# Performance work log

Hardware: AMD Instinct MI355X
Metric: run time of the kernel (lower is better)

Reference implementation:

```python
import jax, jax.numpy as jnp
import numpy as np

N, H, NH, R, E = 50000, 128, 8, 100, 800000
HD = H // NH  # head_dim = 16


def _linear(x, W, b):
    # torch nn.Linear convention: W is [out, in]
    return x @ W.T + b


def _layernorm(x, g, b, eps=1e-5):
    mu = jnp.mean(x, axis=-1, keepdims=True)
    var = jnp.var(x, axis=-1, keepdims=True)
    return (x - mu) * jax.lax.rsqrt(var + eps) * g + b


def setup_inputs() -> dict:
    key = jax.random.key(0)
    ks = jax.random.split(key, 24)
    s = 0.02
    inp = {
        "node_features": jax.random.normal(ks[0], (N, H), jnp.float32),
        "query_embedding": jax.random.normal(ks[1], (1, H), jnp.float32),
        "edge_index": jax.random.randint(ks[2], (2, E), 0, N),
        "edge_type": jax.random.randint(ks[3], (E,), 0, R),
        "relation_embeddings": jax.random.normal(ks[4], (R, H), jnp.float32),
        # attention params
        "Wq": jax.random.normal(ks[5], (H, 2 * H), jnp.float32) * s,
        "bq": jnp.zeros((H,), jnp.float32),
        "Wk": jax.random.normal(ks[6], (H, 2 * H), jnp.float32) * s,
        "bk": jnp.zeros((H,), jnp.float32),
        "Wv": jax.random.normal(ks[7], (H, H), jnp.float32) * s,
        "bv": jnp.zeros((H,), jnp.float32),
        "Wo": jax.random.normal(ks[8], (H, H), jnp.float32) * s,
        "bo": jnp.zeros((H,), jnp.float32),
        # norms
        "n1g": jnp.ones((H,), jnp.float32), "n1b": jnp.zeros((H,), jnp.float32),
        "n2g": jnp.ones((H,), jnp.float32), "n2b": jnp.zeros((H,), jnp.float32),
        # ffn
        "W1": jax.random.normal(ks[9], (4 * H, H), jnp.float32) * s,
        "b1": jnp.zeros((4 * H,), jnp.float32),
        "W2": jax.random.normal(ks[10], (H, 4 * H), jnp.float32) * s,
        "b2": jnp.zeros((H,), jnp.float32),
        # relational layer: 4 interaction transforms stacked [4, H, H]
        "relW": jax.random.normal(ks[11], (4, H, H), jnp.float32) * s,
        "relb": jnp.zeros((4, H), jnp.float32),
        "Wc": jax.random.normal(ks[12], (H, 4 * H), jnp.float32) * s,
        "bc": jnp.zeros((H,), jnp.float32),
        "rng_": jnp.ones((H,), jnp.float32), "rnb": jnp.zeros((H,), jnp.float32),
    }
    return inp


def reference(node_features, query_embedding, edge_index, edge_type, relation_embeddings,
              Wq, bq, Wk, bk, Wv, bv, Wo, bo, n1g, n1b, n2g, n2b,
              W1, b1, W2, b2, relW, relb, Wc, bc, rng_, rnb):
    num_nodes = node_features.shape[0]
    # query-conditioned attention (dropout is identity in eval mode)
    q_exp = jnp.broadcast_to(query_embedding, (num_nodes, H))
    nq = jnp.concatenate([node_features, q_exp], axis=-1)  # [N, 2H]
    q = _linear(nq, Wq, bq).reshape(num_nodes, NH, HD)
    k = _linear(nq, Wk, bk).reshape(num_nodes, NH, HD)
    v = _linear(node_features, Wv, bv).reshape(num_nodes, NH, HD)
    src, dst = edge_index[0], edge_index[1]
    rel_bias = relation_embeddings[edge_type].reshape(-1, NH, HD)  # [E, NH, HD]
    scores = jnp.sum(q[dst] * (k[src] + rel_bias), axis=-1) / np.sqrt(HD)  # [E, NH]
    # sparse softmax over incoming edges per dst node; torch init is zeros with
    # include_self=True amax -> max(0, segment_max)
    seg_max = jnp.maximum(jax.ops.segment_max(scores, dst, num_segments=num_nodes), 0.0)
    exp_s = jnp.exp(scores - seg_max[dst])
    denom = jax.ops.segment_sum(exp_s, dst, num_segments=num_nodes)
    w = exp_s / (denom[dst] + 1e-8)  # [E, NH]
    msg = w[..., None] * v[src]  # [E, NH, HD]
    agg = jax.ops.segment_sum(msg, dst, num_segments=num_nodes).reshape(num_nodes, H)
    attn_out = _linear(agg, Wo, bo)
    x = _layernorm(node_features + attn_out, n1g, n1b)
    ffn = _linear(jax.nn.gelu(_linear(x, W1, b1), approximate=False), W2, b2)
    x = _layernorm(x + ffn, n2g, n2b)
    # relational interaction layer
    t = jnp.einsum('rh,koh->rko', relation_embeddings, relW) + relb  # [R, 4, H]
    combined = t.reshape(relation_embeddings.shape[0], 4 * H)
    rel_out = _layernorm(relation_embeddings + _linear(combined, Wc, bc), rng_, rnb)
    return x, rel_out
```

## Files before the change

kernel.cpp:

```cpp
#include <hip/hip_runtime.h>
#include <hip/hip_bf16.h>
#include <math.h>

using bf16 = __hip_bfloat16;
typedef _Float16 hf;
typedef hf __attribute__((ext_vector_type(2))) hf2;
typedef __attribute__((ext_vector_type(8))) short short8;
typedef __attribute__((ext_vector_type(4))) float floatx4;

__device__ __forceinline__ float b2f(bf16 x){ return __bfloat162float(x); }
__device__ __forceinline__ bf16 f2b(float x){ return __float2bfloat16(x); }
__device__ __forceinline__ short bfbits(float x){ bf16 t = __float2bfloat16(x); return *(short*)&t; }
__device__ __forceinline__ short hfbits(float x){ hf t = (hf)x; return *(short*)&t; }
__device__ __forceinline__ hf2 u2h2(unsigned u){ return *(hf2*)&u; }

__global__ void fill_const(float* __restrict__ p, float v, int n){
  int i = blockIdx.x*blockDim.x + threadIdx.x;
  if (i < n) p[i] = v;
}

__global__ void conv_f2b(const float* __restrict__ src, bf16* __restrict__ dst, int n){
  int i = blockIdx.x*blockDim.x + threadIdx.x;
  if (i < n) dst[i] = f2b(src[i]);
}

__global__ void conv_f2h(const float* __restrict__ src, short* __restrict__ dst, int n){
  int i = blockIdx.x*blockDim.x + threadIdx.x;
  if (i < n) dst[i] = hfbits(src[i]);
}

__global__ void build_wcat(const float* __restrict__ Wq, const float* __restrict__ Wk,
                           const float* __restrict__ Wv, const float* __restrict__ bq,
                           const float* __restrict__ bk, const float* __restrict__ bv,
                           bf16* __restrict__ Wcat, float* __restrict__ bcat){
  int i = blockIdx.x*blockDim.x + threadIdx.x;
  if (i >= 384*256) return;
  int r = i >> 8, c = i & 255;
  float v;
  if (r < 128)       v = Wq[r*256 + c];
  else if (r < 256)  v = Wk[(r-128)*256 + c];
  else               v = (c < 128) ? Wv[(r-256)*128 + c] : 0.f;
  Wcat[i] = f2b(v);
  if (i < 384) bcat[i] = (i < 128) ? bq[i] : (i < 256 ? bk[i-128] : bv[i-256]);
}

__global__ void edge_hist(const int* __restrict__ ei, int E, int* __restrict__ deg){
  int e = blockIdx.x*blockDim.x + threadIdx.x;
  if (e >= E) return;
  atomicAdd(&deg[ei[E + e]], 1);
}

__global__ __launch_bounds__(256) void scan_p1(const int* __restrict__ deg, int Nn,
                                               int* __restrict__ bsum){
  int i = blockIdx.x*256 + threadIdx.x;
  int v = (i < Nn) ? deg[i] : 0;
  #pragma unroll
  for (int off=1; off<64; off<<=1) v += __shfl_xor(v, off);
  __shared__ int ws[4];
  if ((threadIdx.x & 63) == 0) ws[threadIdx.x >> 6] = v;
  __syncthreads();
  if (threadIdx.x == 0) bsum[blockIdx.x] = ws[0] + ws[1] + ws[2] + ws[3];
}

__global__ __launch_bounds__(1024) void scan_p2(int* __restrict__ bsum, int NB, int E,
                                                int* __restrict__ rowptr, int Nn){
  __shared__ int wsum[16];
  __shared__ int carry_s;
  if (threadIdx.x == 0) carry_s = 0;
  __syncthreads();
  const int lane = threadIdx.x & 63, w = threadIdx.x >> 6;
  for (int base = 0; base < NB; base += 1024){
    int i = base + threadIdx.x;
    int v = (i < NB) ? bsum[i] : 0;
    int s = v;
    #pragma unroll
    for (int off=1; off<64; off<<=1){ int t = __shfl_up(s, off); if (lane >= off) s += t; }
    if (lane == 63) wsum[w] = s;
    __syncthreads();
    if (threadIdx.x < 16){
      int ws = wsum[threadIdx.x];
      #pragma unroll
      for (int off=1; off<16; off<<=1){ int t = __shfl_up(ws, off); if (threadIdx.x >= off) ws += t; }
      wsum[threadIdx.x] = ws;
    }
    __syncthreads();
    int carry = carry_s;
    int excl = carry + (w ? wsum[w-1] : 0) + (s - v);
    if (i < NB) bsum[i] = excl;
    __syncthreads();
    if (threadIdx.x == 1023) carry_s = carry + wsum[15];
    __syncthreads();
  }
  if (threadIdx.x == 0) rowptr[Nn] = E;
}

__global__ __launch_bounds__(256) void scan_p3(const int* __restrict__ deg,
      const int* __restrict__ boff, int Nn,
      int* __restrict__ rowptr, int* __restrict__ cursor){
  int i = blockIdx.x*256 + threadIdx.x;
  int v = (i < Nn) ? deg[i] : 0;
  const int lane = threadIdx.x & 63, w = threadIdx.x >> 6;
  int s = v;
  #pragma unroll
  for (int off=1; off<64; off<<=1){ int t = __shfl_up(s, off); if (lane >= off) s += t; }
  __shared__ int wsum[4];
  if (lane == 63) wsum[w] = s;
  __syncthreads();
  int wpre = 0;
  #pragma unroll
  for (int k=0;k<4;k++) if (k < w) wpre += wsum[k];
  int excl = boff[blockIdx.x] + wpre + (s - v);
  if (i < Nn){ rowptr[i] = excl; cursor[i] = excl; }
}

__global__ __launch_bounds__(256) void edge_scatter(const int* __restrict__ ei, const int* __restrict__ ety,
                             int E, int* __restrict__ cursor, unsigned* __restrict__ srcet, int Nn){
  const int p = blockIdx.x & 7;
  const int c = blockIdx.x >> 3;
  const int C = gridDim.x >> 3;
  const int chunk = (Nn + 7) >> 3;
  const int lo = p * chunk;
  const int hi = min(Nn, lo + chunk);
  const int per = (E + C - 1) / C;
  const int e1 = min(E, (c + 1) * per);
  for (int e = c * per + threadIdx.x; e < e1; e += 256){
    int dst = ei[E + e];
    if (dst >= lo && dst < hi){
      int pos = atomicAdd(&cursor[dst], 1);
      srcet[pos] = ((unsigned)ety[e] << 16) | (unsigned)ei[e];
    }
  }
}

__global__ __launch_bounds__(256) void gemm_qkv(const bf16* __restrict__ nfb, const bf16* __restrict__ qeb,
      const bf16* __restrict__ Wcat, const float* __restrict__ bcat,
      short* __restrict__ Qs, short* __restrict__ KVs, int M){
  constexpr int BK=32, LDT=40, K=256;
  __shared__ short As[64*LDT];
  __shared__ short Bs[64*LDT];
  const int tid  = threadIdx.x;
  const int lane = tid & 63;
  const int wave = tid >> 6;
  const int wm = (wave >> 1) * 32, wn = (wave & 1) * 32;
  const long m0 = (long)blockIdx.x * 64;
  const int  n0 = blockIdx.y * 64;
  floatx4 acc00 = {0.f,0.f,0.f,0.f}, acc01 = {0.f,0.f,0.f,0.f};
  floatx4 acc10 = {0.f,0.f,0.f,0.f}, acc11 = {0.f,0.f,0.f,0.f};
  const int srow = tid >> 2, scg = (tid & 3) * 8;
  const int r = lane & 15, q = lane >> 4;
  const short* Ag = (const short*)nfb;
  const short* Qg = (const short*)qeb;
  const short* Bg = (const short*)Wcat;
  for (int k0 = 0; k0 < K; k0 += BK){
    short8 va = {0,0,0,0,0,0,0,0};
    if (k0 < 128){
      long ar = m0 + srow;
      if (ar < M) va = *(const short8*)(Ag + ar*128 + k0 + scg);
    } else {
      va = *(const short8*)(Qg + (k0-128) + scg);
    }
    *(short8*)(&As[srow*LDT + scg]) = va;
    *(short8*)(&Bs[srow*LDT + scg]) = *(const short8*)(Bg + (long)(n0 + srow)*K + k0 + scg);
    __syncthreads();
    short8 a0 = *(const short8*)(&As[(wm      + r)*LDT + q*8]);
    short8 a1 = *(const short8*)(&As[(wm + 16 + r)*LDT + q*8]);
    short8 b0 = *(const short8*)(&Bs[(wn      + r)*LDT + q*8]);
    short8 b1 = *(const short8*)(&Bs[(wn + 16 + r)*LDT + q*8]);
    acc00 = __builtin_amdgcn_mfma_f32_16x16x32_bf16(a0, b0, acc00, 0, 0, 0);
    acc01 = __builtin_amdgcn_mfma_f32_16x16x32_bf16(a0, b1, acc01, 0, 0, 0);
    acc10 = __builtin_amdgcn_mfma_f32_16x16x32_bf16(a1, b0, acc10, 0, 0, 0);
    acc11 = __builtin_amdgcn_mfma_f32_16x16x32_bf16(a1, b1, acc11, 0, 0, 0);
    __syncthreads();
  }
  #pragma unroll
  for (int i=0;i<2;i++)
  #pragma unroll
  for (int j=0;j<2;j++){
    floatx4 av = (i==0) ? ((j==0)?acc00:acc01) : ((j==0)?acc10:acc11);
    int col = n0 + wn + j*16 + r;
    float bsv = bcat[col];
    #pragma unroll
    for (int g=0; g<4; g++){
      long row = m0 + wm + i*16 + q*4 + g;
      if (row < M){
        short bits = hfbits(av[g] + bsv);
        if (col < 128)      Qs[row*128 + col] = bits;
        else if (col < 256){ int d = col - 128; KVs[row*256 + ((d>>1)<<2) + (d&1)] = bits; }
        else               { int d = col - 256; KVs[row*256 + ((d>>1)<<2) + 2 + (d&1)] = bits; }
      }
    }
  }
}

__global__ __launch_bounds__(256) void gemm_bt(const bf16* __restrict__ A, const bf16* __restrict__ B,
      const float* __restrict__ bias, float* __restrict__ C, int M, int N, int K){
  constexpr int BK=32, LDT=40;
  __shared__ short As[64*LDT];
  __shared__ short Bs[64*LDT];
  const int tid  = threadIdx.x;
  const int lane = tid & 63;
  const int wave = tid >> 6;
  const int wm = (wave >> 1) * 32, wn = (wave & 1) * 32;
  const long m0 = (long)blockIdx.x * 64;
  const int  n0 = blockIdx.y * 64;
  floatx4 acc00 = {0.f,0.f,0.f,0.f}, acc01 = {0.f,0.f,0.f,0.f};
  floatx4 acc10 = {0.f,0.f,0.f,0.f}, acc11 = {0.f,0.f,0.f,0.f};
  const int srow = tid >> 2, scg = (tid & 3) * 8;
  const int r = lane & 15, q = lane >> 4;
  const short* Ag = (const short*)A;
  const short* Bg = (const short*)B;
  for (int k0 = 0; k0 < K; k0 += BK){
    short8 va = {0,0,0,0,0,0,0,0};
    long ar = m0 + srow;
    if (ar < M) va = *(const short8*)(Ag + ar*K + k0 + scg);
    *(short8*)(&As[srow*LDT + scg]) = va;
    *(short8*)(&Bs[srow*LDT + scg]) = *(const short8*)(Bg + (long)(n0 + srow)*K + k0 + scg);
    __syncthreads();
    short8 a0 = *(const short8*)(&As[(wm      + r)*LDT + q*8]);
    short8 a1 = *(const short8*)(&As[(wm + 16 + r)*LDT + q*8]);
    short8 b0 = *(const short8*)(&Bs[(wn      + r)*LDT + q*8]);
    short8 b1 = *(const short8*)(&Bs[(wn + 16 + r)*LDT + q*8]);
    acc00 = __builtin_amdgcn_mfma_f32_16x16x32_bf16(a0, b0, acc00, 0, 0, 0);
    acc01 = __builtin_amdgcn_mfma_f32_16x16x32_bf16(a0, b1, acc01, 0, 0, 0);
    acc10 = __builtin_amdgcn_mfma_f32_16x16x32_bf16(a1, b0, acc10, 0, 0, 0);
    acc11 = __builtin_amdgcn_mfma_f32_16x16x32_bf16(a1, b1, acc11, 0, 0, 0);
    __syncthreads();
  }
  #pragma unroll
  for (int i=0;i<2;i++)
  #pragma unroll
  for (int j=0;j<2;j++){
    floatx4 av = (i==0) ? ((j==0)?acc00:acc01) : ((j==0)?acc10:acc11);
    int col = n0 + wn + j*16 + r;
    float bsv = bias[col];
    #pragma unroll
    for (int g=0; g<4; g++){
      long row = m0 + wm + i*16 + q*4 + g;
      if (row < M) C[row*(long)N + col] = av[g] + bsv;
    }
  }
}

__global__ __launch_bounds__(256) void attn_agg(const unsigned* __restrict__ Qh,
     const uint2* __restrict__ KVh, const unsigned* __restrict__ Rh,
     const int* __restrict__ rowptr, const unsigned* __restrict__ srcet,
     unsigned* __restrict__ agg, int Nn){
  const int w = threadIdx.x >> 6, l = threadIdx.x & 63;
  const int n = blockIdx.x*4 + w;
  if (n >= Nn) return;
  hf2 q2 = u2h2(Qh[(long)n*64 + l]);
  int beg = rowptr[n], end = rowptr[n+1];
  float acc0 = 0.f, acc1 = 0.f, denom = 0.f;
  for (int c = beg; c < end; c += 64){
    int cnt = end - c; if (cnt > 64) cnt = 64;
    unsigned se_l = (c + l < end) ? srcet[c + l] : 0u;
    int j = 0;
    for (; j + 4 <= cnt; j += 4){
      unsigned se0 = __shfl(se_l, j+0);
      unsigned se1 = __shfl(se_l, j+1);
      unsigned se2 = __shfl(se_l, j+2);
      unsigned se3 = __shfl(se_l, j+3);
      uint2 kv0 = KVh[(long)(se0 & 0xFFFF)*64 + l];
      uint2 kv1 = KVh[(long)(se1 & 0xFFFF)*64 + l];
      uint2 kv2 = KVh[(long)(se2 & 0xFFFF)*64 + l];
      uint2 kv3 = KVh[(long)(se3 & 0xFFFF)*64 + l];
      unsigned r0 = Rh[(se0 >> 16)*64 + l];
      unsigned r1 = Rh[(se1 >> 16)*64 + l];
      unsigned r2 = Rh[(se2 >> 16)*64 + l];
      unsigned r3 = Rh[(se3 >> 16)*64 + l];
      hf2 kb0 = u2h2(kv0.x) + u2h2(r0);
      hf2 kb1 = u2h2(kv1.x) + u2h2(r1);
      hf2 kb2 = u2h2(kv2.x) + u2h2(r2);
      hf2 kb3 = u2h2(kv3.x) + u2h2(r3);
#if __has_builtin(__builtin_amdgcn_fdot2)
      float p0 = __builtin_amdgcn_fdot2(q2, kb0, 0.f, false);
      float p1 = __builtin_amdgcn_fdot2(q2, kb1, 0.f, false);
      float p2 = __builtin_amdgcn_fdot2(q2, kb2, 0.f, false);
      float p3 = __builtin_amdgcn_fdot2(q2, kb3, 0.f, false);
#else
      float p0 = fmaf((float)q2.y, (float)kb0.y, (float)q2.x * (float)kb0.x);
      float p1 = fmaf((float)q2.y, (float)kb1.y, (float)q2.x * (float)kb1.x);
      float p2 = fmaf((float)q2.y, (float)kb2.y, (float)q2.x * (float)kb2.x);
      float p3 = fmaf((float)q2.y, (float)kb3.y, (float)q2.x * (float)kb3.x);
#endif
      p0 += __shfl_xor(p0, 1); p1 += __shfl_xor(p1, 1);
      p2 += __shfl_xor(p2, 1); p3 += __shfl_xor(p3, 1);
      p0 += __shfl_xor(p0, 2); p1 += __shfl_xor(p1, 2);
      p2 += __shfl_xor(p2, 2); p3 += __shfl_xor(p3, 2);
      p0 += __shfl_xor(p0, 4); p1 += __shfl_xor(p1, 4);
      p2 += __shfl_xor(p2, 4); p3 += __shfl_xor(p3, 4);
      float e0 = __expf(p0 * 0.25f);
      float e1 = __expf(p1 * 0.25f);
      float e2 = __expf(p2 * 0.25f);
      float e3 = __expf(p3 * 0.25f);
      denom += e0; denom += e1; denom += e2; denom += e3;
      hf2 v0 = u2h2(kv0.y), v1 = u2h2(kv1.y), v2 = u2h2(kv2.y), v3 = u2h2(kv3.y);
      acc0 = fmaf(e0, (float)v0.x, acc0);
      acc1 = fmaf(e0, (float)v0.y, acc1);
      acc0 = fmaf(e1, (float)v1.x, acc0);
      acc1 = fmaf(e1, (float)v1.y, acc1);
      acc0 = fmaf(e2, (float)v2.x, acc0);
      acc1 = fmaf(e2, (float)v2.y, acc1);
      acc0 = fmaf(e3, (float)v3.x, acc0);
      acc1 = fmaf(e3, (float)v3.y, acc1);
    }
    for (; j < cnt; ++j){
      unsigned se = __shfl(se_l, j);
      int src = se & 0xFFFF;
      int et  = se >> 16;
      uint2 kv = KVh[(long)src*64 + l];
      hf2 kb = u2h2(kv.x) + u2h2(Rh[et*64 + l]);
#if __has_builtin(__builtin_amdgcn_fdot2)
      float p = __builtin_amdgcn_fdot2(q2, kb, 0.f, false);
#else
      float p = fmaf((float)q2.y, (float)kb.y, (float)q2.x * (float)kb.x);
#endif
      p += __shfl_xor(p, 1); p += __shfl_xor(p, 2); p += __shfl_xor(p, 4);
      float es = __expf(p * 0.25f);
      denom += es;
      hf2 v2 = u2h2(kv.y);
      acc0 = fmaf(es, (float)v2.x, acc0);
      acc1 = fmaf(es, (float)v2.y, acc1);
    }
  }
  float inv = 1.f / (denom + 1e-8f);
  unsigned out = ((unsigned)(unsigned short)bfbits(acc1 * inv) << 16)
               |  (unsigned)(unsigned short)bfbits(acc0 * inv);
  agg[(long)n*64 + l] = out;
}

__global__ __launch_bounds__(128) void ln_add1(const float* __restrict__ nf, const float* __restrict__ attn,
     const float* __restrict__ g, const float* __restrict__ b, bf16* __restrict__ xout){
  long n = blockIdx.x; int t = threadIdx.x;
  float y = nf[n*128 + t] + attn[n*128 + t];
  float s = y, s2 = y*y;
  #pragma unroll
  for (int off=32; off>0; off>>=1){ s += __shfl_xor(s, off); s2 += __shfl_xor(s2, off); }
  __shared__ float ps[4];
  if ((t & 63) == 0){ ps[(t>>6)*2] = s; ps[(t>>6)*2+1] = s2; }
  __syncthreads();
  float tot = ps[0] + ps[2], tot2 = ps[1] + ps[3];
  float mu = tot * (1.f/128.f);
  float var = tot2 * (1.f/128.f) - mu*mu;
  float rs = rsqrtf(var + 1e-5f);
  xout[n*128 + t] = f2b((y - mu)*rs*g[t] + b[t]);
}

__global__ __launch_bounds__(256) void ffn_fused(const bf16* __restrict__ X, const bf16* __restrict__ W1,
    const float* __restrict__ b1, const bf16* __restrict__ W2, const float* __restrict__ b2,
    float* __restrict__ Out, int M){
  __shared__ short Xs[64*136];
  __shared__ short Hs[64*140];
  __shared__ short Ws[64*136];
  const int tid = threadIdx.x, lane = tid & 63, wave = tid >> 6;
  const int r = lane & 15, q = lane >> 4;
  const int wm = (wave >> 1) * 32, wn = (wave & 1) * 32;
  const long m0 = (long)blockIdx.x * 64;
  const short* Xg  = (const short*)X;
  const short* W1g = (const short*)W1;
  const short* W2g = (const short*)W2;
  #pragma unroll
  for (int c=0;c<4;c++){
    int idx = c*256 + tid, row = idx >> 4, ch = (idx & 15) * 8;
    short8 v = {0,0,0,0,0,0,0,0};
    long ar = m0 + row;
    if (ar < M) v = *(const short8*)(Xg + ar*128 + ch);
    *(short8*)(&Xs[row*136 + ch]) = v;
  }
  const int wn2 = (wave & 1) * 64;
  floatx4 o[2][4];
  #pragma unroll
  for (int i=0;i<2;i++)
  #pragma unroll
  for (int j=0;j<4;j++) o[i][j] = (floatx4){0.f,0.f,0.f,0.f};
  for (int qtr = 0; qtr < 4; ++qtr){
    const int hb = qtr * 128;
    for (int c0 = 0; c0 < 128; c0 += 64){
      #pragma unroll
      for (int c=0;c<4;c++){
        int idx = c*256 + tid, row = idx >> 4, ch = (idx & 15) * 8;
        *(short8*)(&Ws[row*136 + ch]) = *(const short8*)(W1g + (long)(hb + c0 + row)*128 + ch);
      }
      __syncthreads();
      floatx4 h00 = {0.f,0.f,0.f,0.f}, h01 = {0.f,0.f,0.f,0.f};
      floatx4 h10 = {0.f,0.f,0.f,0.f}, h11 = {0.f,0.f,0.f,0.f};
      #pragma unroll
      for (int k0 = 0; k0 < 128; k0 += 32){
        short8 a0 = *(const short8*)(&Xs[(wm      + r)*136 + k0 + q*8]);
        short8 a1 = *(const short8*)(&Xs[(wm + 16 + r)*136 + k0 + q*8]);
        short8 b0 = *(const short8*)(&Ws[(wn      + r)*136 + k0 + q*8]);
        short8 bv = *(const short8*)(&Ws[(wn + 16 + r)*136 + k0 + q*8]);
        h00 = __builtin_amdgcn_mfma_f32_16x16x32_bf16(a0, b0, h00, 0, 0, 0);
        h01 = __builtin_amdgcn_mfma_f32_16x16x32_bf16(a0, bv, h01, 0, 0, 0);
        h10 = __builtin_amdgcn_mfma_f32_16x16x32_bf16(a1, b0, h10, 0, 0, 0);
        h11 = __builtin_amdgcn_mfma_f32_16x16x32_bf16(a1, bv, h11, 0, 0, 0);
      }
      #pragma unroll
      for (int i=0;i<2;i++)
      #pragma unroll
      for (int j=0;j<2;j++){
        floatx4 av = (i==0) ? ((j==0)?h00:h01) : ((j==0)?h10:h11);
        int col = wn + j*16 + r;
        float bb = b1[hb + c0 + col];
        #pragma unroll
        for (int g=0; g<4; g++){
          int row = wm + i*16 + q*4 + g;
          float v = av[g] + bb;
          v = 0.5f * v * (1.f + erff(v * 0.70710678118f));
          Hs[row*140 + c0 + col] = bfbits(v);
        }
      }
      __syncthreads();
    }
    for (int k0 = 0; k0 < 128; k0 += 64){
      #pragma unroll
      for (int c=0;c<4;c++){
        int idx = c*256 + tid, row = idx >> 3, ch = (idx & 7) * 8;
        *(short8*)(&Ws[row*68 + ch]) = *(const short8*)(W2g + (long)row*512 + hb + k0 + ch);
      }
      __syncthreads();
      #pragma unroll
      for (int ks = 0; ks < 64; ks += 32){
        short8 a0 = *(const short8*)(&Hs[(wm      + r)*140 + k0 + ks + q*8]);
        short8 a1 = *(const short8*)(&Hs[(wm + 16 + r)*140 + k0 + ks + q*8]);
        #pragma unroll
        for (int j=0;j<4;j++){
          short8 bj = *(const short8*)(&Ws[(wn2 + j*16 + r)*68 + ks + q*8]);
          o[0][j] = __builtin_amdgcn_mfma_f32_16x16x32_bf16(a0, bj, o[0][j], 0, 0, 0);
          o[1][j] = __builtin_amdgcn_mfma_f32_16x16x32_bf16(a1, bj, o[1][j], 0, 0, 0);
        }
      }
      __syncthreads();
    }
  }
  #pragma unroll
  for (int i=0;i<2;i++)
  #pragma unroll
  for (int j=0;j<4;j++){
    int col = wn2 + j*16 + r;
    float bb = b2[col];
    #pragma unroll
    for (int g=0; g<4; g++){
      long row = m0 + wm + i*16 + q*4 + g;
      if (row < M) Out[row*128 + col] = o[i][j][g] + bb;
    }
  }
}

__global__ __launch_bounds__(128) void ln_add2(const bf16* __restrict__ X, const float* __restrict__ ffo,
     const float* __restrict__ g, const float* __restrict__ b, float* __restrict__ out){
  long n = blockIdx.x; int t = threadIdx.x;
  float y = b2f(X[n*128 + t]) + ffo[n*128 + t];
  float s = y, s2 = y*y;
  #pragma unroll
  for (int off=32; off>0; off>>=1){ s += __shfl_xor(s, off); s2 += __shfl_xor(s2, off); }
  __shared__ float ps[4];
  if ((t & 63) == 0){ ps[(t>>6)*2] = s; ps[(t>>6)*2+1] = s2; }
  __syncthreads();
  float tot = ps[0] + ps[2], tot2 = ps[1] + ps[3];
  float mu = tot * (1.f/128.f);
  float var = tot2 * (1.f/128.f) - mu*mu;
  float rs = rsqrtf(var + 1e-5f);
  out[n*128 + t] = (y - mu)*rs*g[t] + b[t];
}

__device__ __forceinline__ float dotf(const float* __restrict__ s, const float* __restrict__ w, int n){
  float acc = 0.f;
  const float4* w4 = (const float4*)w;
  #pragma unroll 4
  for (int j = 0; j < (n >> 2); ++j){
    float4 wv = w4[j];
    acc += s[4*j]*wv.x + s[4*j+1]*wv.y + s[4*j+2]*wv.z + s[4*j+3]*wv.w;
  }
  return acc;
}

__global__ __launch_bounds__(128) void rel_layer(const float* __restrict__ rel, const float* __restrict__ relW,
    const float* __restrict__ relb, const float* __restrict__ Wc, const float* __restrict__ bc,
    const float* __restrict__ gn, const float* __restrict__ bn, float* __restrict__ out){
  int rr = blockIdx.x, t = threadIdx.x;
  __shared__ float rrow[128];
  __shared__ float comb[512];
  rrow[t] = rel[(long)rr*128 + t];
  __syncthreads();
  #pragma unroll
  for (int k=0;k<4;k++){
    comb[k*128 + t] = dotf(rrow, relW + ((long)(k*128) + t)*128, 128) + relb[k*128 + t];
  }
  __syncthreads();
  float c2 = dotf(comb, Wc + (long)t*512, 512) + bc[t];
  float y = rrow[t] + c2;
  float s = y, s2 = y*y;
  #pragma unroll
  for (int off=32; off>0; off>>=1){ s += __shfl_xor(s, off); s2 += __shfl_xor(s2, off); }
  __shared__ float ps[4];
  if ((t & 63) == 0){ ps[(t>>6)*2] = s; ps[(t>>6)*2+1] = s2; }
  __syncthreads();
  float tot = ps[0] + ps[2], tot2 = ps[1] + ps[3];
  float mu = tot * (1.f/128.f);
  float var = tot2 * (1.f/128.f) - mu*mu;
  float rs = rsqrtf(var + 1e-5f);
  out[(long)rr*128 + t] = (y - mu)*rs*gn[t] + bn[t];
}

extern "C" void kernel_launch(void* const* d_in, const int* in_sizes, int n_in,
                              void* d_out, int out_size, void* d_ws, size_t ws_size,
                              hipStream_t stream){
  const int H = 128;
  auto S = [&](int i){ return in_sizes[i]; };
  bool ok = (n_in == 27);
  if (ok){
    ok = ok && S(1)==H && (S(0)%H)==0 && S(2)==2*S(3) && (S(4)%H)==0;
    ok = ok && S(5)==2*H*H && S(7)==2*H*H && S(9)==H*H && S(11)==H*H;
    ok = ok && S(17)==4*H*H && S(19)==4*H*H && S(21)==4*H*H && S(23)==4*H*H;
    ok = ok && out_size == S(0) + S(4);
  }
  if (!ok){
    fill_const<<<(out_size + 255)/256, 256, 0, stream>>>((float*)d_out, 100.0f, out_size);
    return;
  }

  const float* nf   = (const float*)d_in[0];
  const float* qe   = (const float*)d_in[1];
  const int*   ei   = (const int*)  d_in[2];
  const int*   ety  = (const int*)  d_in[3];
  const float* rel  = (const float*)d_in[4];
  const float* Wq   = (const float*)d_in[5];
  const float* bq   = (const float*)d_in[6];
  const float* Wk   = (const float*)d_in[7];
  const float* bk   = (const float*)d_in[8];
  const float* Wv   = (const float*)d_in[9];
  const float* bv   = (const float*)d_in[10];
  const float* Wo   = (const float*)d_in[11];
  const float* bo   = (const float*)d_in[12];
  const float* n1g  = (const float*)d_in[13];
  const float* n1b  = (const float*)d_in[14];
  const float* n2g  = (const float*)d_in[15];
  const float* n2b  = (const float*)d_in[16];
  const float* W1   = (const float*)d_in[17];
  const float* b1   = (const float*)d_in[18];
  const float* W2   = (const float*)d_in[19];
  const float* b2v  = (const float*)d_in[20];
  const float* relW = (const float*)d_in[21];
  const float* relbp= (const float*)d_in[22];
  const float* Wc   = (const float*)d_in[23];
  const float* bc   = (const float*)d_in[24];
  const float* rng  = (const float*)d_in[25];
  const float* rnb  = (const float*)d_in[26];

  const int N = in_sizes[0] / 128;
  const int E = in_sizes[2] / 2;
  const int R = in_sizes[4] / 128;

  char* ws = (char*)d_ws;
  size_t off = 0;
  auto alloc = [&](size_t bytes)->char*{
    char* p = ws + off; off = (off + bytes + 255) & ~(size_t)255; return p;
  };
  char*     regNA  = alloc((size_t)N * 256);
  char*     regKV  = alloc((size_t)N * 512);
  unsigned* Qh     = (unsigned*)alloc((size_t)N * 256);
  bf16*     xlb    = (bf16*)    alloc((size_t)N * 256);
  bf16*     qeb    = (bf16*)    alloc(256);
  bf16*     Wcat   = (bf16*)    alloc((size_t)384*256*2);
  float*    bcat   = (float*)   alloc(384*4);
  bf16*     Wob    = (bf16*)    alloc((size_t)128*128*2);
  bf16*     W1b    = (bf16*)    alloc((size_t)512*128*2);
  bf16*     W2b    = (bf16*)    alloc((size_t)128*512*2);
  short*    Rh     = (short*)   alloc((size_t)R*128*2);
  int*      deg    = (int*)     alloc((size_t)N * 4);
  int*      rowptr = (int*)     alloc((size_t)(N+1) * 4);
  int*      cursor = (int*)     alloc((size_t)N * 4);
  unsigned* srcet  = (unsigned*)alloc((size_t)E * 4);
  const int NB = (N + 255) / 256;
  int*      bsum   = (int*)     alloc((size_t)NB * 4);

  if (off > ws_size){
    fill_const<<<(out_size + 255)/256, 256, 0, stream>>>((float*)d_out, 50.0f, out_size);
    return;
  }

  bf16*     nfb  = (bf16*)regNA;
  unsigned* aggp = (unsigned*)regNA;
  uint2*    KVh  = (uint2*)regKV;
  float*    attn = (float*)regKV;
  float*    ffo  = (float*)regKV;
  float*    outx = (float*)d_out;
  float*    outr = (float*)d_out + (size_t)N*128;

  conv_f2b<<<(N*128 + 255)/256, 256, 0, stream>>>(nf, nfb, N*128);
  conv_f2b<<<1, 128, 0, stream>>>(qe, qeb, 128);
  build_wcat<<<(384*256 + 255)/256, 256, 0, stream>>>(Wq, Wk, Wv, bq, bk, bv, Wcat, bcat);
  conv_f2b<<<(128*128 + 255)/256, 256, 0, stream>>>(Wo, Wob, 128*128);
  conv_f2b<<<(512*128 + 255)/256, 256, 0, stream>>>(W1, W1b, 512*128);
  conv_f2b<<<(128*512 + 255)/256, 256, 0, stream>>>(W2, W2b, 128*512);
  conv_f2h<<<(R*128 + 255)/256, 256, 0, stream>>>(rel, Rh, R*128);

  hipMemsetAsync(deg, 0, (size_t)N*4, stream);
  edge_hist<<<(E + 255)/256, 256, 0, stream>>>(ei, E, deg);
  scan_p1<<<NB, 256, 0, stream>>>(deg, N, bsum);
  scan_p2<<<1, 1024, 0, stream>>>(bsum, NB, E, rowptr, N);
  scan_p3<<<NB, 256, 0, stream>>>(deg, bsum, N, rowptr, cursor);
  edge_scatter<<<2048, 256, 0, stream>>>(ei, ety, E, cursor, srcet, N);

  dim3 g1((N + 63)/64, 6);
  gemm_qkv<<<g1, 256, 0, stream>>>(nfb, qeb, Wcat, bcat, (short*)Qh, (short*)KVh, N);
  attn_agg<<<(N + 3)/4, 256, 0, stream>>>(Qh, KVh, (const unsigned*)Rh, rowptr, srcet, aggp, N);
  dim3 g2((N + 63)/64, 2);
  gemm_bt<<<g2, 256, 0, stream>>>((const bf16*)aggp, Wob, bo, attn, N, 128, 128);
  ln_add1<<<N, 128, 0, stream>>>(nf, attn, n1g, n1b, xlb);
  ffn_fused<<<(N + 63)/64, 256, 0, stream>>>(xlb, W1b, b1, W2b, b2v, ffo, N);
  ln_add2<<<N, 128, 0, stream>>>(xlb, ffo, n2g, n2b, outx);
  rel_layer<<<R, 128, 0, stream>>>(rel, relW, relbp, Wc, bc, rng, rnb, outr);
}
```

Baseline: 443.4 us.

## Fuse residual-add LayerNorms into the output-projection and FFN GEMM epilogues

New measurement: 426.6 us. -3.8%, faster.

```diff
diff --git a/kernel.cpp b/kernel.cpp
--- a/kernel.cpp
+++ b/kernel.cpp
@@ -192,51 +192,108 @@
   }
 }
 
-__global__ __launch_bounds__(256) void gemm_bt(const bf16* __restrict__ A, const bf16* __restrict__ B,
-      const float* __restrict__ bias, float* __restrict__ C, int M, int N, int K){
-  constexpr int BK=32, LDT=40;
-  __shared__ short As[64*LDT];
-  __shared__ short Bs[64*LDT];
-  const int tid  = threadIdx.x;
-  const int lane = tid & 63;
-  const int wave = tid >> 6;
-  const int wm = (wave >> 1) * 32, wn = (wave & 1) * 32;
+__global__ __launch_bounds__(256) void gemm_bt_ln(const bf16* __restrict__ A, const bf16* __restrict__ B,
+      const float* __restrict__ bias, const float* __restrict__ nf,
+      const float* __restrict__ gam, const float* __restrict__ bet,
+      bf16* __restrict__ xout, int M){
+  __shared__ short As[64*136];
+  __shared__ short Bs[128*136];
+  const int tid = threadIdx.x, lane = tid & 63, wave = tid >> 6;
+  const int r = lane & 15, q = lane >> 4;
+  const int wm = (wave >> 1) * 32, wn2 = (wave & 1) * 64;
   const long m0 = (long)blockIdx.x * 64;
-  const int  n0 = blockIdx.y * 64;
-  floatx4 acc00 = {0.f,0.f,0.f,0.f}, acc01 = {0.f,0.f,0.f,0.f};
-  floatx4 acc10 = {0.f,0.f,0.f,0.f}, acc11 = {0.f,0.f,0.f,0.f};
-  const int srow = tid >> 2, scg = (tid & 3) * 8;
-  const int r = lane & 15, q = lane >> 4;
   const short* Ag = (const short*)A;
   const short* Bg = (const short*)B;
-  for (int k0 = 0; k0 < K; k0 += BK){
-    short8 va = {0,0,0,0,0,0,0,0};
-    long ar = m0 + srow;
-    if (ar < M) va = *(const short8*)(Ag + ar*K + k0 + scg);
-    *(short8*)(&As[srow*LDT + scg]) = va;
-    *(short8*)(&Bs[srow*LDT + scg]) = *(const short8*)(Bg + (long)(n0 + srow)*K + k0 + scg);
-    __syncthreads();
-    short8 a0 = *(const short8*)(&As[(wm      + r)*LDT + q*8]);
-    short8 a1 = *(const short8*)(&As[(wm + 16 + r)*LDT + q*8]);
-    short8 b0 = *(const short8*)(&Bs[(wn      + r)*LDT + q*8]);
-    short8 b1 = *(const short8*)(&Bs[(wn + 16 + r)*LDT + q*8]);
-    acc00 = __builtin_amdgcn_mfma_f32_16x16x32_bf16(a0, b0, acc00, 0, 0, 0);
-    acc01 = __builtin_amdgcn_mfma_f32_16x16x32_bf16(a0, b1, acc01, 0, 0, 0);
-    acc10 = __builtin_amdgcn_mfma_f32_16x16x32_bf16(a1, b0, acc10, 0, 0, 0);
-    acc11 = __builtin_amdgcn_mfma_f32_16x16x32_bf16(a1, b1, acc11, 0, 0, 0);
-    __syncthreads();
-  }
+  #pragma unroll
+  for (int c=0;c<4;c++){
+    int idx = c*256 + tid, row = idx >> 4, ch = (idx & 15) * 8;
+    short8 v = {0,0,0,0,0,0,0,0};
+    long ar = m0 + row;
+    if (ar < M) v = *(const short8*)(Ag + ar*128 + ch);
+    *(short8*)(&As[row*136 + ch]) = v;
+  }
+  #pragma unroll
+  for (int c=0;c<8;c++){
+    int idx = c*256 + tid, row = idx >> 4, ch = (idx & 15) * 8;
+    *(short8*)(&Bs[row*136 + ch]) = *(const short8*)(Bg + (long)row*128 + ch);
+  }
+  __syncthreads();
+  floatx4 o[2][4];
   #pragma unroll
   for (int i=0;i<2;i++)
   #pragma unroll
-  for (int j=0;j<2;j++){
-    floatx4 av = (i==0) ? ((j==0)?acc00:acc01) : ((j==0)?acc10:acc11);
-    int col = n0 + wn + j*16 + r;
-    float bsv = bias[col];
+  for (int j=0;j<4;j++) o[i][j] = (floatx4){0.f,0.f,0.f,0.f};
+  #pragma unroll
+  for (int k0 = 0; k0 < 128; k0 += 32){
+    short8 a0 = *(const short8*)(&As[(wm      + r)*136 + k0 + q*8]);
+    short8 a1 = *(const short8*)(&As[(wm + 16 + r)*136 + k0 + q*8]);
+    #pragma unroll
+    for (int j=0;j<4;j++){
+      short8 bj = *(const short8*)(&Bs[(wn2 + j*16 + r)*136 + k0 + q*8]);
+      o[0][j] = __builtin_amdgcn_mfma_f32_16x16x32_bf16(a0, bj, o[0][j], 0, 0, 0);
+      o[1][j] = __builtin_amdgcn_mfma_f32_16x16x32_bf16(a1, bj, o[1][j], 0, 0, 0);
+    }
+  }
+  __syncthreads();
+  float* redp = (float*)Bs;
+  float* stat = redp + 256;
+  float yv[2][4][4];
+  #pragma unroll
+  for (int i=0;i<2;i++){
+    #pragma unroll
+    for (int j=0;j<4;j++){
+      int col = wn2 + j*16 + r;
+      float bsv = bias[col];
+      #pragma unroll
+      for (int g=0; g<4; g++){
+        int row = wm + i*16 + q*4 + g;
+        long grow = m0 + row;
+        float nfv = (grow < M) ? nf[grow*128 + col] : 0.f;
+        yv[i][j][g] = o[i][j][g] + bsv + nfv;
+      }
+    }
+  }
+  #pragma unroll
+  for (int i=0;i<2;i++){
     #pragma unroll
     for (int g=0; g<4; g++){
-      long row = m0 + wm + i*16 + q*4 + g;
-      if (row < M) C[row*(long)N + col] = av[g] + bsv;
+      float s  = yv[i][0][g] + yv[i][1][g] + yv[i][2][g] + yv[i][3][g];
+      float s2 = yv[i][0][g]*yv[i][0][g] + yv[i][1][g]*yv[i][1][g]
+               + yv[i][2][g]*yv[i][2][g] + yv[i][3][g]*yv[i][3][g];
+      #pragma unroll
+      for (int m=1; m<16; m<<=1){ s += __shfl_xor(s, m); s2 += __shfl_xor(s2, m); }
+      if (r == 0){
+        int row = wm + i*16 + q*4 + g;
+        redp[row*4 + (wave & 1)*2 + 0] = s;
+        redp[row*4 + (wave & 1)*2 + 1] = s2;
+      }
+    }
+  }
+  __syncthreads();
+  if (tid < 64){
+    float s  = redp[tid*4 + 0] + redp[tid*4 + 2];
+    float s2 = redp[tid*4 + 1] + redp[tid*4 + 3];
+    float mu = s * (1.f/128.f);
+    float var = s2 * (1.f/128.f) - mu*mu;
+    stat[tid*2 + 0] = mu;
+    stat[tid*2 + 1] = rsqrtf(var + 1e-5f);
+  }
+  __syncthreads();
+  #pragma unroll
+  for (int i=0;i<2;i++){
+    #pragma unroll
+    for (int j=0;j<4;j++){
+      int col = wn2 + j*16 + r;
+      float gv = gam[col], bv = bet[col];
+      #pragma unroll
+      for (int g=0; g<4; g++){
+        int row = wm + i*16 + q*4 + g;
+        long grow = m0 + row;
+        if (grow < M){
+          float mu = stat[row*2], rs = stat[row*2 + 1];
+          xout[grow*128 + col] = f2b((yv[i][j][g] - mu)*rs*gv + bv);
+        }
+      }
     }
   }
 }
@@ -329,25 +386,9 @@
   agg[(long)n*64 + l] = out;
 }
 
-__global__ __launch_bounds__(128) void ln_add1(const float* __restrict__ nf, const float* __restrict__ attn,
-     const float* __restrict__ g, const float* __restrict__ b, bf16* __restrict__ xout){
-  long n = blockIdx.x; int t = threadIdx.x;
-  float y = nf[n*128 + t] + attn[n*128 + t];
-  float s = y, s2 = y*y;
-  #pragma unroll
-  for (int off=32; off>0; off>>=1){ s += __shfl_xor(s, off); s2 += __shfl_xor(s2, off); }
-  __shared__ float ps[4];
-  if ((t & 63) == 0){ ps[(t>>6)*2] = s; ps[(t>>6)*2+1] = s2; }
-  __syncthreads();
-  float tot = ps[0] + ps[2], tot2 = ps[1] + ps[3];
-  float mu = tot * (1.f/128.f);
-  float var = tot2 * (1.f/128.f) - mu*mu;
-  float rs = rsqrtf(var + 1e-5f);
-  xout[n*128 + t] = f2b((y - mu)*rs*g[t] + b[t]);
-}
-
 __global__ __launch_bounds__(256) void ffn_fused(const bf16* __restrict__ X, const bf16* __restrict__ W1,
     const float* __restrict__ b1, const bf16* __restrict__ W2, const float* __restrict__ b2,
+    const float* __restrict__ gam, const float* __restrict__ bet,
     float* __restrict__ Out, int M){
   __shared__ short Xs[64*136];
   __shared__ short Hs[64*140];
@@ -433,35 +474,66 @@
       __syncthreads();
     }
   }
-  #pragma unroll
-  for (int i=0;i<2;i++)
-  #pragma unroll
-  for (int j=0;j<4;j++){
-    int col = wn2 + j*16 + r;
-    float bb = b2[col];
+  float* redp = (float*)Ws;
+  float* stat = redp + 256;
+  float yv[2][4][4];
+  #pragma unroll
+  for (int i=0;i<2;i++){
+    #pragma unroll
+    for (int j=0;j<4;j++){
+      int col = wn2 + j*16 + r;
+      float bb = b2[col];
+      #pragma unroll
+      for (int g=0; g<4; g++){
+        int row = wm + i*16 + q*4 + g;
+        float xr = b2f(*(const bf16*)&Xs[row*136 + col]);
+        yv[i][j][g] = o[i][j][g] + bb + xr;
+      }
+    }
+  }
+  #pragma unroll
+  for (int i=0;i<2;i++){
     #pragma unroll
     for (int g=0; g<4; g++){
-      long row = m0 + wm + i*16 + q*4 + g;
-      if (row < M) Out[row*128 + col] = o[i][j][g] + bb;
-    }
-  }
-}
-
-__global__ __launch_bounds__(128) void ln_add2(const bf16* __restrict__ X, const float* __restrict__ ffo,
-     const float* __restrict__ g, const float* __restrict__ b, float* __restrict__ out){
-  long n = blockIdx.x; int t = threadIdx.x;
-  float y = b2f(X[n*128 + t]) + ffo[n*128 + t];
-  float s = y, s2 = y*y;
-  #pragma unroll
-  for (int off=32; off>0; off>>=1){ s += __shfl_xor(s, off); s2 += __shfl_xor(s2, off); }
-  __shared__ float ps[4];
-  if ((t & 63) == 0){ ps[(t>>6)*2] = s; ps[(t>>6)*2+1] = s2; }
-  __syncthreads();
-  float tot = ps[0] + ps[2], tot2 = ps[1] + ps[3];
-  float mu = tot * (1.f/128.f);
-  float var = tot2 * (1.f/128.f) - mu*mu;
-  float rs = rsqrtf(var + 1e-5f);
-  out[n*128 + t] = (y - mu)*rs*g[t] + b[t];
+      float s  = yv[i][0][g] + yv[i][1][g] + yv[i][2][g] + yv[i][3][g];
+      float s2 = yv[i][0][g]*yv[i][0][g] + yv[i][1][g]*yv[i][1][g]
+               + yv[i][2][g]*yv[i][2][g] + yv[i][3][g]*yv[i][3][g];
+      #pragma unroll
+      for (int m=1; m<16; m<<=1){ s += __shfl_xor(s, m); s2 += __shfl_xor(s2, m); }
+      if (r == 0){
+        int row = wm + i*16 + q*4 + g;
+        redp[row*4 + (wave & 1)*2 + 0] = s;
+        redp[row*4 + (wave & 1)*2 + 1] = s2;
+      }
+    }
+  }
+  __syncthreads();
+  if (tid < 64){
+    float s  = redp[tid*4 + 0] + redp[tid*4 + 2];
+    float s2 = redp[tid*4 + 1] + redp[tid*4 + 3];
+    float mu = s * (1.f/128.f);
+    float var = s2 * (1.f/128.f) - mu*mu;
+    stat[tid*2 + 0] = mu;
+    stat[tid*2 + 1] = rsqrtf(var + 1e-5f);
+  }
+  __syncthreads();
+  #pragma unroll
+  for (int i=0;i<2;i++){
+    #pragma unroll
+    for (int j=0;j<4;j++){
+      int col = wn2 + j*16 + r;
+      float gv = gam[col], bv = bet[col];
+      #pragma unroll
+      for (int g=0; g<4; g++){
+        int row = wm + i*16 + q*4 + g;
+        long grow = m0 + row;
+        if (grow < M){
+          float mu = stat[row*2], rs = stat[row*2 + 1];
+          Out[grow*128 + col] = (yv[i][j][g] - mu)*rs*gv + bv;
+        }
+      }
+    }
+  }
 }
 
 __device__ __forceinline__ float dotf(const float* __restrict__ s, const float* __restrict__ w, int n){
@@ -583,8 +655,6 @@
   bf16*     nfb  = (bf16*)regNA;
   unsigned* aggp = (unsigned*)regNA;
   uint2*    KVh  = (uint2*)regKV;
-  float*    attn = (float*)regKV;
-  float*    ffo  = (float*)regKV;
   float*    outx = (float*)d_out;
   float*    outr = (float*)d_out + (size_t)N*128;
 
@@ -606,10 +676,7 @@
   dim3 g1((N + 63)/64, 6);
   gemm_qkv<<<g1, 256, 0, stream>>>(nfb, qeb, Wcat, bcat, (short*)Qh, (short*)KVh, N);
   attn_agg<<<(N + 3)/4, 256, 0, stream>>>(Qh, KVh, (const unsigned*)Rh, rowptr, srcet, aggp, N);
-  dim3 g2((N + 63)/64, 2);
-  gemm_bt<<<g2, 256, 0, stream>>>((const bf16*)aggp, Wob, bo, attn, N, 128, 128);
-  ln_add1<<<N, 128, 0, stream>>>(nf, attn, n1g, n1b, xlb);
-  ffn_fused<<<(N + 63)/64, 256, 0, stream>>>(xlb, W1b, b1, W2b, b2v, ffo, N);
-  ln_add2<<<N, 128, 0, stream>>>(xlb, ffo, n2g, n2b, outx);
+  gemm_bt_ln<<<(N + 63)/64, 256, 0, stream>>>((const bf16*)aggp, Wob, bo, nf, n1g, n1b, xlb, N);
+  ffn_fused<<<(N + 63)/64, 256, 0, stream>>>(xlb, W1b, b1, W2b, b2v, n2g, n2b, outx, N);
   rel_layer<<<R, 128, 0, stream>>>(rel, relW, relbp, Wc, bc, rng, rnb, outr);
 }
```
